# Optimization experiments

Measured on AMD Instinct MI355X. Metric: run time of the kernel, lower is better.

Reference implementation:

```python
import jax, jax.numpy as jnp
import numpy as np

EPS = 1e-8  # torch F.cosine_similarity default eps


def setup_inputs() -> dict:
    key = jax.random.key(0)
    k1, k2, k3, k4 = jax.random.split(key, 4)
    B, S, D_in, D_e, E = 4, 128, 768, 256, 100000
    return {
        "x": jax.random.normal(k1, (B, S, D_in), dtype=jnp.float32),
        "W": jax.random.normal(k2, (D_e, D_in), dtype=jnp.float32) * 0.02,
        "b": jax.random.normal(k3, (D_e,), dtype=jnp.float32) * 0.02,
        "entity_embedding": jax.random.normal(k4, (E, D_e), dtype=jnp.float32),
    }


def reference(x, W, b, entity_embedding):
    # Linear projection + tanh: [B,S,D_e]
    q = jnp.tanh(jnp.einsum('bsi,ei->bse', x, W) + b)
    # Cosine similarity = L2-normalize both sides, then GEMM (fused; avoids
    # the [B,S,E,D] broadcast intermediate of the original).
    qn = q / jnp.maximum(jnp.linalg.norm(q, axis=-1, keepdims=True), EPS)
    en = entity_embedding / jnp.maximum(
        jnp.linalg.norm(entity_embedding, axis=-1, keepdims=True), EPS)
    return jnp.einsum('bsd,ed->bse', qn, en)  # [B,S,E]
```

## Files before the change

### kernel.cpp

```cpp
#include <hip/hip_runtime.h>
#include <hip/hip_bf16.h>

#define D_IN  768
#define D_E   256
#define M_TOT 512
#define E_TOT 100000

typedef __attribute__((ext_vector_type(4))) float f32x4;
typedef __attribute__((ext_vector_type(8))) short bf16x8;

__device__ __forceinline__ unsigned short bf16bits(float f) {
    union { __hip_bfloat16 h; unsigned short u; } c;
    c.h = __float2bfloat16(f);
    return c.u;
}

__device__ __forceinline__ void gload_lds16(const void* g, void* l) {
    __builtin_amdgcn_global_load_lds(
        (const __attribute__((address_space(1))) void*)g,
        (__attribute__((address_space(3))) void*)l, 16, 0, 0);
}

#define PROJ_BLOCKS 64
#define PREP_BLOCKS 1563
#define PP_GRID (PROJ_BLOCKS + PREP_BLOCKS)
#define PTM 8
#define PBK 64
#define PROUNDS (D_IN / PBK)

__global__ __launch_bounds__(512) void fused_pp(
    const float* __restrict__ x, const float* __restrict__ W,
    const float* __restrict__ b, const float* __restrict__ en,
    unsigned short* __restrict__ qb, unsigned short* __restrict__ eb)
{
    __shared__ float ws[D_E * (PBK + 1)];
    __shared__ float xs[PTM][PBK];
    __shared__ float red[PTM][4];
    __shared__ float qiv[PTM];

    const int t   = threadIdx.x;
    const int bid = blockIdx.x;

    if (bid >= PROJ_BLOCKS) {
        const int lane = t & 63;
        const int gw   = (bid - PROJ_BLOCKS) * 8 + (t >> 6);
        #pragma unroll 2
        for (int i = 0; i < 8; ++i) {
            const int row = gw * 8 + i;
            if (row >= E_TOT) break;
            const float4 v = *reinterpret_cast<const float4*>(
                en + (size_t)row * D_E + lane * 4);
            float s = v.x*v.x + v.y*v.y + v.z*v.z + v.w*v.w;
            #pragma unroll
            for (int off = 1; off < 64; off <<= 1) s += __shfl_xor(s, off, 64);
            const float sc = 1.0f / fmaxf(sqrtf(s), 1e-8f);
            union { unsigned short u[4]; uint2 d; } o;
            o.u[0] = bf16bits(v.x * sc); o.u[1] = bf16bits(v.y * sc);
            o.u[2] = bf16bits(v.z * sc); o.u[3] = bf16bits(v.w * sc);
            *reinterpret_cast<uint2*>(eb + (size_t)row * D_E + lane * 4) = o.d;
        }
        return;
    }

    const int m0   = bid * PTM;
    const int e    = t & 255;
    const int half = t >> 8;
    const int c4   = t & 15;
    const int rr   = t >> 4;

    float4 wreg[8];
    float  xreg = 0.f;
    float  acc[4] = {0.f, 0.f, 0.f, 0.f};

    #pragma unroll
    for (int i = 0; i < 8; ++i)
        wreg[i] = *reinterpret_cast<const float4*>(
            &W[(size_t)(i * 32 + rr) * D_IN + c4 * 4]);
    xreg = x[(size_t)(m0 + (t >> 6)) * D_IN + (t & 63)];

    for (int rd = 0; rd < PROUNDS; ++rd) {
        #pragma unroll
        for (int i = 0; i < 8; ++i) {
            float* dst = &ws[(i * 32 + rr) * (PBK + 1) + c4 * 4];
            dst[0] = wreg[i].x; dst[1] = wreg[i].y;
            dst[2] = wreg[i].z; dst[3] = wreg[i].w;
        }
        xs[t >> 6][t & 63] = xreg;
        __syncthreads();
        if (rd + 1 < PROUNDS) {
            const int k0 = (rd + 1) * PBK;
            #pragma unroll
            for (int i = 0; i < 8; ++i)
                wreg[i] = *reinterpret_cast<const float4*>(
                    &W[(size_t)(i * 32 + rr) * D_IN + k0 + c4 * 4]);
            xreg = x[(size_t)(m0 + (t >> 6)) * D_IN + k0 + (t & 63)];
        }
        #pragma unroll
        for (int k = 0; k < PBK; ++k) {
            const float wv = ws[e * (PBK + 1) + k];
            #pragma unroll
            for (int j = 0; j < 4; ++j)
                acc[j] = fmaf(xs[half * 4 + j][k], wv, acc[j]);
        }
        __syncthreads();
    }

    const float bias = b[e];
    const int wv4 = (t >> 6) & 3;
    const int lane = t & 63;
    float q[4];
    #pragma unroll
    for (int j = 0; j < 4; ++j) {
        q[j] = tanhf(acc[j] + bias);
        float s = q[j] * q[j];
        #pragma unroll
        for (int off = 1; off < 64; off <<= 1) s += __shfl_xor(s, off, 64);
        if (lane == 0) red[half * 4 + j][wv4] = s;
    }
    __syncthreads();
    if (t < PTM) {
        const float s = red[t][0] + red[t][1] + red[t][2] + red[t][3];
        qiv[t] = 1.0f / fmaxf(sqrtf(s), 1e-8f);
    }
    __syncthreads();
    #pragma unroll
    for (int j = 0; j < 4; ++j)
        qb[(size_t)(m0 + half * 4 + j) * D_E + e] =
            bf16bits(q[j] * qiv[half * 4 + j]);
}

#define BM 128
#define BN 64
#define TPB 25
#define NGRPN 63
#define SIM_GRID (NGRPN * (M_TOT / BM))

__global__ __launch_bounds__(512, 2) void sim_kernel(
    const unsigned short* __restrict__ eb, const unsigned short* __restrict__ qb,
    float* __restrict__ out)
{
    __shared__ unsigned short qs[BM * D_E];
    __shared__ unsigned short es[2][BN * D_E];

    const int t    = threadIdx.x;
    const int lane = t & 63;
    const int wid  = t >> 6;
    const int l15  = lane & 15;
    const int lk   = lane >> 4;
    const int wm   = (wid >> 1) * 32;
    const int wn   = (wid & 1) * 32;

    int vbid;
    {
        const int q = SIM_GRID >> 3, r = SIM_GRID & 7;
        const int xcd = blockIdx.x & 7, rk = blockIdx.x >> 3;
        vbid = (xcd < r ? xcd * (q + 1) : r * (q + 1) + (xcd - r) * q) + rk;
    }
    const int mg    = vbid & 3;
    const int ngrp  = vbid >> 2;
    const int m0    = mg * BM;
    const int nbase = ngrp * (TPB * BN);

    #pragma unroll
    for (int i = 0; i < 8; ++i) {
        const int c   = i * 512 + t;
        const int row = c >> 5;
        const int c16 = c & 31;
        const unsigned short* src =
            qb + (size_t)(m0 + row) * D_E + ((c16 ^ (row & 7)) << 3);
        gload_lds16(src, (void*)&qs[(size_t)c << 3]);
    }
    #pragma unroll
    for (int i = 0; i < 4; ++i) {
        const int c   = i * 512 + t;
        const int row = c >> 5;
        const int c16 = c & 31;
        int rg = nbase + row; if (rg >= E_TOT) rg = E_TOT - 1;
        const unsigned short* src =
            eb + (size_t)rg * D_E + ((c16 ^ (row & 7)) << 3);
        gload_lds16(src, (void*)&es[0][(size_t)c << 3]);
    }

    const char* qsb = reinterpret_cast<const char*>(qs);

    for (int tt = 0; tt < TPB; ++tt) {
        const int n0 = nbase + tt * BN;
        if (n0 >= E_TOT) break;

        if (tt == 0) {
            asm volatile("s_waitcnt vmcnt(0)" ::: "memory");
        } else {
            asm volatile("s_waitcnt vmcnt(4)" ::: "memory");
        }
        __builtin_amdgcn_s_barrier();
        __builtin_amdgcn_sched_barrier(0);

        const int cur = tt & 1;
        const int nn0 = n0 + BN;
        if (tt + 1 < TPB && nn0 < E_TOT) {
            #pragma unroll
            for (int i = 0; i < 4; ++i) {
                const int c   = i * 512 + t;
                const int row = c >> 5;
                const int c16 = c & 31;
                int rg = nn0 + row; if (rg >= E_TOT) rg = E_TOT - 1;
                const unsigned short* src =
                    eb + (size_t)rg * D_E + ((c16 ^ (row & 7)) << 3);
                gload_lds16(src, (void*)&es[cur ^ 1][(size_t)c << 3]);
            }
        }

        const char* esb = reinterpret_cast<const char*>(&es[cur][0]);

        f32x4 acc[2][2];
        #pragma unroll
        for (int mf = 0; mf < 2; ++mf)
            #pragma unroll
            for (int nf = 0; nf < 2; ++nf)
                acc[mf][nf] = (f32x4){0.f, 0.f, 0.f, 0.f};

        __builtin_amdgcn_s_setprio(1);
        #pragma unroll
        for (int ks = 0; ks < 8; ++ks) {
            const int kb = ks * 64 + lk * 16;
            bf16x8 ef[2];
            #pragma unroll
            for (int nf = 0; nf < 2; ++nf) {
                const int row = wn + nf * 16 + l15;
                const int cb  = kb ^ ((row & 7) << 4);
                ef[nf] = *reinterpret_cast<const bf16x8*>(esb + row * 512 + cb);
            }
            #pragma unroll
            for (int mf = 0; mf < 2; ++mf) {
                const int rq  = wm + mf * 16 + l15;
                const int cbq = kb ^ ((rq & 7) << 4);
                const bf16x8 qf =
                    *reinterpret_cast<const bf16x8*>(qsb + rq * 512 + cbq);
                acc[mf][0] = __builtin_amdgcn_mfma_f32_16x16x32_bf16(
                    ef[0], qf, acc[mf][0], 0, 0, 0);
                acc[mf][1] = __builtin_amdgcn_mfma_f32_16x16x32_bf16(
                    ef[1], qf, acc[mf][1], 0, 0, 0);
            }
        }
        __builtin_amdgcn_s_setprio(0);

        #pragma unroll
        for (int mf = 0; mf < 2; ++mf) {
            const int m = m0 + wm + mf * 16 + l15;
            #pragma unroll
            for (int nf = 0; nf < 2; ++nf) {
                const int n = n0 + wn + nf * 16 + lk * 4;
                if (n < E_TOT)
                    *reinterpret_cast<f32x4*>(&out[(size_t)m * E_TOT + n]) =
                        acc[mf][nf];
            }
        }
    }
}

extern "C" void kernel_launch(void* const* d_in, const int* in_sizes, int n_in,
                              void* d_out, int out_size, void* d_ws, size_t ws_size,
                              hipStream_t stream) {
    const float* x  = (const float*)d_in[0];
    const float* W  = (const float*)d_in[1];
    const float* b  = (const float*)d_in[2];
    const float* en = (const float*)d_in[3];
    float* out = (float*)d_out;

    unsigned short* qb = (unsigned short*)d_ws;
    unsigned short* eb = (unsigned short*)((char*)d_ws + (size_t)M_TOT * D_E * 2);

    fused_pp<<<PP_GRID, 512, 0, stream>>>(x, W, b, en, qb, eb);
    sim_kernel<<<SIM_GRID, 512, 0, stream>>>(eb, qb, out);
}
```

Measured before the change: 131.3 us.

## Keep query fragments in registers and reuse LDS for entity double buffer

The query tile is loaded once from LDS into registers (16 bf16x8 fragments per lane), so the LDS region that held it can be reused for the entity double buffer. This shrinks shared memory to 64KB per block, which lets the launch bounds ask for 4 blocks per CU. The grid is doubled, with half as many entity tiles per block, to add parallelism. The cost is higher register pressure under the tighter launch bound, which risks spills, and more blocks each loading the query tile.

After: 128.0 us. 1.03x faster.

```diff
diff --git a/kernel.cpp b/kernel.cpp
--- a/kernel.cpp
+++ b/kernel.cpp
@@ -131,16 +131,15 @@
 
 #define BM 128
 #define BN 64
-#define TPB 25
-#define NGRPN 63
-#define SIM_GRID (NGRPN * (M_TOT / BM))
-
-__global__ __launch_bounds__(512, 2) void sim_kernel(
+#define TPB 13
+#define NGRPN 126
+#define SIM_GRID (NGRPN * 4)
+
+__global__ __launch_bounds__(512, 4) void sim_kernel(
     const unsigned short* __restrict__ eb, const unsigned short* __restrict__ qb,
     float* __restrict__ out)
 {
-    __shared__ unsigned short qs[BM * D_E];
-    __shared__ unsigned short es[2][BN * D_E];
+    __shared__ unsigned short pool[32768];
 
     const int t    = threadIdx.x;
     const int lane = t & 63;
@@ -161,56 +160,76 @@
     const int m0    = mg * BM;
     const int nbase = ngrp * (TPB * BN);
 
+    if (nbase >= E_TOT) return;
+
+    int nt = (E_TOT - nbase + BN - 1) / BN;
+    if (nt > TPB) nt = TPB;
+
     #pragma unroll
     for (int i = 0; i < 8; ++i) {
         const int c   = i * 512 + t;
         const int row = c >> 5;
         const int c16 = c & 31;
-        const unsigned short* src =
-            qb + (size_t)(m0 + row) * D_E + ((c16 ^ (row & 7)) << 3);
-        gload_lds16(src, (void*)&qs[(size_t)c << 3]);
-    }
+        gload_lds16(qb + (size_t)(m0 + row) * D_E + ((c16 ^ (row & 7)) << 3),
+                    (void*)&pool[(size_t)c << 3]);
+    }
+    asm volatile("s_waitcnt vmcnt(0)" ::: "memory");
+    __builtin_amdgcn_sched_barrier(0);
+    __builtin_amdgcn_s_barrier();
+    __builtin_amdgcn_sched_barrier(0);
+
+    const char* qsb = reinterpret_cast<const char*>(pool);
+    bf16x8 qf[2][8];
+    #pragma unroll
+    for (int mf = 0; mf < 2; ++mf) {
+        const int rq = wm + mf * 16 + l15;
+        #pragma unroll
+        for (int ks = 0; ks < 8; ++ks) {
+            const int cb = (ks * 64 + lk * 16) ^ ((rq & 7) << 4);
+            qf[mf][ks] = *reinterpret_cast<const bf16x8*>(qsb + rq * 512 + cb);
+        }
+    }
+    asm volatile("s_waitcnt lgkmcnt(0)" ::: "memory");
+    __builtin_amdgcn_sched_barrier(0);
+    __builtin_amdgcn_s_barrier();
+    __builtin_amdgcn_sched_barrier(0);
+
     #pragma unroll
     for (int i = 0; i < 4; ++i) {
         const int c   = i * 512 + t;
         const int row = c >> 5;
         const int c16 = c & 31;
         int rg = nbase + row; if (rg >= E_TOT) rg = E_TOT - 1;
-        const unsigned short* src =
-            eb + (size_t)rg * D_E + ((c16 ^ (row & 7)) << 3);
-        gload_lds16(src, (void*)&es[0][(size_t)c << 3]);
-    }
-
-    const char* qsb = reinterpret_cast<const char*>(qs);
-
-    for (int tt = 0; tt < TPB; ++tt) {
+        gload_lds16(eb + (size_t)rg * D_E + ((c16 ^ (row & 7)) << 3),
+                    (void*)&pool[(size_t)c << 3]);
+    }
+
+    for (int tt = 0; tt < nt; ++tt) {
         const int n0 = nbase + tt * BN;
-        if (n0 >= E_TOT) break;
-
-        if (tt == 0) {
-            asm volatile("s_waitcnt vmcnt(0)" ::: "memory");
-        } else {
-            asm volatile("s_waitcnt vmcnt(4)" ::: "memory");
-        }
+
+        if (tt == 0) asm volatile("s_waitcnt vmcnt(0)" ::: "memory");
+        else         asm volatile("s_waitcnt vmcnt(4)" ::: "memory");
         __builtin_amdgcn_s_barrier();
         __builtin_amdgcn_sched_barrier(0);
 
         const int cur = tt & 1;
-        const int nn0 = n0 + BN;
-        if (tt + 1 < TPB && nn0 < E_TOT) {
+        unsigned short* escur = pool + (cur ? 16384 : 0);
+        unsigned short* esnxt = pool + (cur ? 0 : 16384);
+
+        if (tt + 1 < nt) {
+            const int nn0 = n0 + BN;
             #pragma unroll
             for (int i = 0; i < 4; ++i) {
                 const int c   = i * 512 + t;
                 const int row = c >> 5;
                 const int c16 = c & 31;
                 int rg = nn0 + row; if (rg >= E_TOT) rg = E_TOT - 1;
-                const unsigned short* src =
-                    eb + (size_t)rg * D_E + ((c16 ^ (row & 7)) << 3);
-                gload_lds16(src, (void*)&es[cur ^ 1][(size_t)c << 3]);
-            }
-        }
-
-        const char* esb = reinterpret_cast<const char*>(&es[cur][0]);
+                gload_lds16(eb + (size_t)rg * D_E + ((c16 ^ (row & 7)) << 3),
+                            (void*)&esnxt[(size_t)c << 3]);
+            }
+        }
+
+        const char* esb = reinterpret_cast<const char*>(escur);
 
         f32x4 acc[2][2];
         #pragma unroll
@@ -232,14 +251,10 @@
             }
             #pragma unroll
             for (int mf = 0; mf < 2; ++mf) {
-                const int rq  = wm + mf * 16 + l15;
-                const int cbq = kb ^ ((rq & 7) << 4);
-                const bf16x8 qf =
-                    *reinterpret_cast<const bf16x8*>(qsb + rq * 512 + cbq);
                 acc[mf][0] = __builtin_amdgcn_mfma_f32_16x16x32_bf16(
-                    ef[0], qf, acc[mf][0], 0, 0, 0);
+                    ef[0], qf[mf][ks], acc[mf][0], 0, 0, 0);
                 acc[mf][1] = __builtin_amdgcn_mfma_f32_16x16x32_bf16(
-                    ef[1], qf, acc[mf][1], 0, 0, 0);
+                    ef[1], qf[mf][ks], acc[mf][1], 0, 0, 0);
             }
         }
         __builtin_amdgcn_s_setprio(0);
```
